# Optimization experiments

Hardware: AMD Instinct MI355X
Metric: run time of the kernel (lower is better)

Reference implementation:

```python
import jax, jax.numpy as jnp
import numpy as np

B, T = 64, 1024
VOCAB, EMBED, HIDDEN = 55, 64, 128


def setup_inputs() -> dict:
    key = jax.random.key(0)
    ks = jax.random.split(key, 15)
    stdv = 1.0 / np.sqrt(HIDDEN)
    u = lambda k, s: jax.random.uniform(k, s, jnp.float32, -stdv, stdv)
    return {
        "x": jax.random.randint(ks[0], (B, T), 0, VOCAB),
        "emb": jax.random.normal(ks[1], (VOCAB, EMBED), jnp.float32),
        "w_ih0": u(ks[2], (HIDDEN, EMBED)),
        "b_ih0": u(ks[3], (HIDDEN,)),
        "w_hh0": u(ks[4], (HIDDEN, HIDDEN)),
        "b_hh0": u(ks[5], (HIDDEN,)),
        "w_ih1": u(ks[6], (HIDDEN, HIDDEN)),
        "b_ih1": u(ks[7], (HIDDEN,)),
        "w_hh1": u(ks[8], (HIDDEN, HIDDEN)),
        "b_hh1": u(ks[9], (HIDDEN,)),
        "attn_w": u(ks[10], (HIDDEN, HIDDEN)),
        "attn_b": u(ks[11], (HIDDEN,)),
        "fc_w": u(ks[12], (VOCAB, 2 * HIDDEN)),
        "fc_b": u(ks[13], (VOCAB,)),
    }


def reference(x, emb, w_ih0, b_ih0, w_hh0, b_hh0, w_ih1, b_ih1, w_hh1, b_hh1,
              attn_w, attn_b, fc_w, fc_b):
    Bx, Tx = x.shape
    H = w_hh0.shape[0]
    e = emb[x]  # [B, T, E]

    def step(carry, x_t):  # x_t: [B, E]
        h0, h1 = carry
        h0 = jnp.tanh(x_t @ w_ih0.T + b_ih0 + h0 @ w_hh0.T + b_hh0)
        h1 = jnp.tanh(h0 @ w_ih1.T + b_ih1 + h1 @ w_hh1.T + b_hh1)
        return (h0, h1), h1

    init = (jnp.zeros((Bx, H), e.dtype), jnp.zeros((Bx, H), e.dtype))
    _, outs = jax.lax.scan(step, init, jnp.swapaxes(e, 0, 1))  # [T, B, H]
    outs = jnp.swapaxes(outs, 0, 1)  # [B, T, H]

    Q = outs @ attn_w.T + attn_b  # [B, T, H]
    scores = jnp.einsum('bth,bsh->bts', Q, outs) / jnp.sqrt(jnp.asarray(H, e.dtype))
    causal = jnp.tril(jnp.ones((Tx, Tx), bool))  # [T, T]
    scores = jnp.where(causal[None], scores, jnp.asarray(-jnp.inf, scores.dtype))
    attn = jax.nn.softmax(scores, axis=-1)
    context = jnp.einsum('bts,bsh->bth', attn, outs)  # [B, T, H]

    combined = jnp.concatenate([outs, context], axis=-1)  # [B, T, 2H]
    logits = combined @ fc_w.T + fc_b  # [B, T, vocab]
    return logits
```

## Files before the change

kernel.cpp:

```cpp
#include <hip/hip_runtime.h>
#include <hip/hip_bf16.h>
#include <cstdint>
#include <cstddef>


typedef __attribute__((ext_vector_type(8))) short short8;
typedef __attribute__((ext_vector_type(4))) float f32x4;

__device__ __forceinline__ float bf2f(unsigned short u) {
    union { unsigned int i; float f; } c; c.i = ((unsigned int)u) << 16; return c.f;
}
__device__ __forceinline__ unsigned short f2bf(float f) {
    union { float f; unsigned int i; } c; c.f = f;
    unsigned int u = c.i;
    u += 0x7fffu + ((u >> 16) & 1u);
    return (unsigned short)(u >> 16);
}
__device__ __forceinline__ unsigned int pk_bf16(float lo, float hi) {
    union { __hip_bfloat162 h2; unsigned int u; } c;
    c.h2 = __float22bfloat162_rn(make_float2(lo, hi));
    return c.u;
}
__device__ __forceinline__ float fast_tanh(float x) {
    float e = __expf(2.0f * x);
    return 1.0f - 2.0f * __builtin_amdgcn_rcpf(e + 1.0f);
}
__device__ __forceinline__ void bar_lds() {
    asm volatile("s_waitcnt lgkmcnt(0)\n\ts_barrier" ::: "memory");
}
__device__ __forceinline__ short8 ld_a_bf16(const float* p) {
    const float4* q = (const float4*)p;
    float4 f0 = q[0], f1 = q[1];
    short8 r;
    r[0]=(short)f2bf(f0.x); r[1]=(short)f2bf(f0.y);
    r[2]=(short)f2bf(f0.z); r[3]=(short)f2bf(f0.w);
    r[4]=(short)f2bf(f1.x); r[5]=(short)f2bf(f1.y);
    r[6]=(short)f2bf(f1.z); r[7]=(short)f2bf(f1.w);
    return r;
}
__device__ __forceinline__ void ld_fc_hilo(const float* p, short8& hi, short8& lo) {
    const float4* q = (const float4*)p;
    float4 f0 = q[0], f1 = q[1];
    float ff[8] = {f0.x, f0.y, f0.z, f0.w, f1.x, f1.y, f1.z, f1.w};
#pragma unroll
    for (int i = 0; i < 8; ++i) {
        unsigned short hb = f2bf(ff[i]);
        hi[i] = (short)hb;
        lo[i] = (short)f2bf(ff[i] - bf2f(hb));
    }
}

__global__ __launch_bounds__(128)
void k_we(const float* __restrict__ emb, const float* __restrict__ w_ih0,
          const float* __restrict__ b_ih0, const float* __restrict__ b_hh0,
          float* __restrict__ WE)
{
    __shared__ float ev[64];
    const int i = threadIdx.x;
    const int v = blockIdx.x;
    if (i < 64) ev[i] = emb[v * 64 + i];
    __syncthreads();
    float s = b_ih0[i] + b_hh0[i];
    const float* wr = w_ih0 + i * 64;
#pragma unroll
    for (int k = 0; k < 64; ++k) s += wr[k] * ev[k];
    WE[v * 128 + i] = s;
}

__global__ __launch_bounds__(256)
void k_weg(const int* __restrict__ x, const float* __restrict__ WE,
           float* __restrict__ WEg)
{
    __shared__ int xv[32];
    const int tid = threadIdx.x;
    const int b   = blockIdx.y;
    const int t0  = blockIdx.x * 32;
    if (tid < 32) xv[tid] = x[b * 1024 + t0 + tid];
    __syncthreads();
#pragma unroll
    for (int it = 0; it < 4; ++it) {
        int tt = it * 8 + (tid >> 5);
        int c4 = tid & 31;
        float4 v = ((const float4*)(WE + xv[tt] * 128))[c4];
        ((float4*)(WEg + ((size_t)b * 1024 + t0 + tt) * 128))[c4] = v;
    }
}

__global__ __launch_bounds__(512, 1)
void k_scan5(const float* __restrict__ WEg,
             const float* __restrict__ w_hh0,
             const float* __restrict__ w_ih1, const float* __restrict__ b_ih1,
             const float* __restrict__ w_hh1, const float* __restrict__ b_hh1,
             unsigned short* __restrict__ outs_bf)
{
    const int tid   = threadIdx.x;
    const int w     = tid >> 6;
    const int lane  = tid & 63;
    const int quad  = lane >> 4;
    const int n     = lane & 15;
    const int bbase = blockIdx.x * 16;

    __shared__ __align__(16) unsigned short h0buf[2][16][136];
    __shared__ __align__(16) unsigned short h1buf[2][16][136];

    if (w < 4) {
        const int r0 = w * 32 + quad * 4;
        const int r1 = r0 + 16;
        short8 a0[2][4];
#pragma unroll
        for (int r = 0; r < 2; ++r) {
            const size_t mrow = (size_t)(w * 32 + r * 16 + n) * 128;
#pragma unroll
            for (int ks = 0; ks < 4; ++ks)
                a0[r][ks] = ld_a_bf16(w_hh0 + mrow + ks * 32 + quad * 8);
        }
        const size_t wegB0 = (size_t)(bbase + n) * 131072 + r0;
        const size_t wegB1 = wegB0 + 16;
        {
            float4 p0 = *(const float4*)(WEg + wegB0);
            float4 p1 = *(const float4*)(WEg + wegB1);
            *(uint2*)&h0buf[0][n][r0] = make_uint2(
                pk_bf16(fast_tanh(p0.x), fast_tanh(p0.y)),
                pk_bf16(fast_tanh(p0.z), fast_tanh(p0.w)));
            *(uint2*)&h0buf[0][n][r1] = make_uint2(
                pk_bf16(fast_tanh(p1.x), fast_tanh(p1.y)),
                pk_bf16(fast_tanh(p1.z), fast_tanh(p1.w)));
        }
        float4 wA0 = *(const float4*)(WEg + wegB0 + 128);
        float4 wA1 = *(const float4*)(WEg + wegB1 + 128);
        float4 wB0 = *(const float4*)(WEg + wegB0 + 256);
        float4 wB1 = *(const float4*)(WEg + wegB1 + 256);
        float4 wC0 = *(const float4*)(WEg + wegB0 + 384);
        float4 wC1 = *(const float4*)(WEg + wegB1 + 384);
        __syncthreads();

        for (int t = 0; t < 1024; ++t) {
            const int p = t & 1;
            if (t < 1023) {
                const unsigned short* h0p = &h0buf[p][n][quad * 8];
                short8 bh[4];
#pragma unroll
                for (int ks = 0; ks < 4; ++ks)
                    bh[ks] = *(const short8*)(h0p + ks * 32);
                f32x4 c0 = (f32x4){wA0.x, wA0.y, wA0.z, wA0.w};
                f32x4 c1 = (f32x4){wA1.x, wA1.y, wA1.z, wA1.w};
#pragma unroll
                for (int ks = 0; ks < 4; ++ks) {
                    c0 = __builtin_amdgcn_mfma_f32_16x16x32_bf16(a0[0][ks], bh[ks], c0, 0,0,0);
                    c1 = __builtin_amdgcn_mfma_f32_16x16x32_bf16(a0[1][ks], bh[ks], c1, 0,0,0);
                }
                wA0 = wB0; wA1 = wB1; wB0 = wC0; wB1 = wC1;
                const size_t tpre = (size_t)((t + 4 < 1024) ? t + 4 : 1023) * 128;
                wC0 = *(const float4*)(WEg + wegB0 + tpre);
                wC1 = *(const float4*)(WEg + wegB1 + tpre);
                *(uint2*)&h0buf[p ^ 1][n][r0] = make_uint2(
                    pk_bf16(fast_tanh(c0[0]), fast_tanh(c0[1])),
                    pk_bf16(fast_tanh(c0[2]), fast_tanh(c0[3])));
                *(uint2*)&h0buf[p ^ 1][n][r1] = make_uint2(
                    pk_bf16(fast_tanh(c1[0]), fast_tanh(c1[1])),
                    pk_bf16(fast_tanh(c1[2]), fast_tanh(c1[3])));
            }
            bar_lds();
        }
    } else {
        const int w2 = w - 4;
        const int r0 = w2 * 32 + quad * 4;
        const int r1 = r0 + 16;
        short8 a1[2][4], a2[2][4];
#pragma unroll
        for (int r = 0; r < 2; ++r) {
            const size_t mrow = (size_t)(w2 * 32 + r * 16 + n) * 128;
#pragma unroll
            for (int ks = 0; ks < 4; ++ks) {
                a1[r][ks] = ld_a_bf16(w_ih1 + mrow + ks * 32 + quad * 8);
                a2[r][ks] = ld_a_bf16(w_hh1 + mrow + ks * 32 + quad * 8);
            }
        }
        f32x4 b1i[2];
#pragma unroll
        for (int r = 0; r < 2; ++r)
#pragma unroll
            for (int j = 0; j < 4; ++j) {
                int row = w2 * 32 + r * 16 + quad * 4 + j;
                b1i[r][j] = b_ih1[row] + b_hh1[row];
            }
        *(uint2*)&h1buf[0][n][r0] = make_uint2(0u, 0u);
        *(uint2*)&h1buf[0][n][r1] = make_uint2(0u, 0u);
        unsigned short* outp0 = outs_bf + (size_t)(bbase + n) * 131072 + r0;
        unsigned short* outp1 = outp0 + 16;
        __syncthreads();

        for (int t = 0; t < 1024; ++t) {
            const int p = t & 1;
            const unsigned short* h0p = &h0buf[p][n][quad * 8];
            const unsigned short* h1p = &h1buf[p][n][quad * 8];
            short8 bh0[4], bh1[4];
#pragma unroll
            for (int ks = 0; ks < 4; ++ks) {
                bh0[ks] = *(const short8*)(h0p + ks * 32);
                bh1[ks] = *(const short8*)(h1p + ks * 32);
            }
            f32x4 c0 = b1i[0], c1 = b1i[1];
            f32x4 d0 = (f32x4){0.f,0.f,0.f,0.f}, d1 = (f32x4){0.f,0.f,0.f,0.f};
#pragma unroll
            for (int ks = 0; ks < 4; ++ks) {
                c0 = __builtin_amdgcn_mfma_f32_16x16x32_bf16(a1[0][ks], bh0[ks], c0, 0,0,0);
                c1 = __builtin_amdgcn_mfma_f32_16x16x32_bf16(a1[1][ks], bh0[ks], c1, 0,0,0);
                d0 = __builtin_amdgcn_mfma_f32_16x16x32_bf16(a2[0][ks], bh1[ks], d0, 0,0,0);
                d1 = __builtin_amdgcn_mfma_f32_16x16x32_bf16(a2[1][ks], bh1[ks], d1, 0,0,0);
            }
            uint2 o0 = make_uint2(
                pk_bf16(fast_tanh(c0[0] + d0[0]), fast_tanh(c0[1] + d0[1])),
                pk_bf16(fast_tanh(c0[2] + d0[2]), fast_tanh(c0[3] + d0[3])));
            uint2 o1 = make_uint2(
                pk_bf16(fast_tanh(c1[0] + d1[0]), fast_tanh(c1[1] + d1[1])),
                pk_bf16(fast_tanh(c1[2] + d1[2]), fast_tanh(c1[3] + d1[3])));
            *(uint2*)&h1buf[p ^ 1][n][r0] = o0;
            *(uint2*)&h1buf[p ^ 1][n][r1] = o1;
            *(uint2*)(outp0 + (size_t)t * 128) = o0;
            *(uint2*)(outp1 + (size_t)t * 128) = o1;
            bar_lds();
        }
    }
}

__global__ __launch_bounds__(256)
void k_transpose(const unsigned short* __restrict__ outs_bf,
                 unsigned short* __restrict__ outsT)
{
    __shared__ unsigned short lt[128][130];
    const int tid = threadIdx.x;
    const int t0  = blockIdx.x * 128;
    const int b   = blockIdx.y;
    const unsigned int* src =
        (const unsigned int*)(outs_bf + ((size_t)b * 1024 + t0) * 128);
    for (int idx = tid; idx < 8192; idx += 256) {
        int tr = idx >> 6, h2 = idx & 63;
        unsigned int v = src[tr * 64 + h2];
        lt[tr][h2 * 2]     = (unsigned short)(v & 0xffffu);
        lt[tr][h2 * 2 + 1] = (unsigned short)(v >> 16);
    }
    __syncthreads();
    unsigned int* dst = (unsigned int*)(outsT + (size_t)b * 128 * 1024);
    for (int idx = tid; idx < 8192; idx += 256) {
        int h = idx >> 6, t2 = idx & 63;
        unsigned int v = (unsigned int)lt[t2 * 2][h] |
                         ((unsigned int)lt[t2 * 2 + 1][h] << 16);
        dst[h * 512 + (t0 >> 1) + t2] = v;
    }
}

__global__ __launch_bounds__(512, 1)
void k_attnfc(const unsigned short* __restrict__ outs_bf,
              const unsigned short* __restrict__ outsT,
              const float* __restrict__ attn_w, const float* __restrict__ attn_b,
              const float* __restrict__ fc_w, const float* __restrict__ fc_b,
              float* __restrict__ out)
{
    __shared__ __align__(16) unsigned char smem[100352];
    unsigned short* lK = (unsigned short*)smem;
    unsigned short* lV = (unsigned short*)(smem + 32768);
    unsigned short* lP = (unsigned short*)(smem + 65536);

    const int tid  = threadIdx.x;
    const int w    = tid >> 6;
    const int lane = tid & 63;
    const int quad = lane >> 4;
    const int n    = lane & 15;
    const int qt   = blockIdx.x;
    const int b    = blockIdx.y;
    unsigned short* lPw = lP + w * 2176;
    const float cscale = 0.08838834764831845f;

    const unsigned short* outsB = outs_bf + (size_t)b * 131072;
    const int qrow = qt * 128 + w * 16 + n;

    short8 bo[4];
#pragma unroll
    for (int ks = 0; ks < 4; ++ks)
        bo[ks] = *(const short8*)(outsB + (size_t)qrow * 128 + ks * 32 + quad * 8);
#pragma unroll
    for (int mt = 0; mt < 8; ++mt) {
        short8 aw[4];
#pragma unroll
        for (int ks = 0; ks < 4; ++ks)
            aw[ks] = ld_a_bf16(attn_w + (size_t)(mt * 16 + n) * 128 + ks * 32 + quad * 8);
        f32x4 cq;
#pragma unroll
        for (int r = 0; r < 4; ++r) cq[r] = attn_b[mt * 16 + quad * 4 + r];
#pragma unroll
        for (int ks = 0; ks < 4; ++ks)
            cq = __builtin_amdgcn_mfma_f32_16x16x32_bf16(aw[ks], bo[ks], cq, 0,0,0);
        *(uint2*)&lPw[n * 136 + mt * 16 + quad * 4] =
            make_uint2(pk_bf16(cq[0], cq[1]), pk_bf16(cq[2], cq[3]));
    }
    short8 qf[4];
#pragma unroll
    for (int ks = 0; ks < 4; ++ks)
        qf[ks] = *(const short8*)&lPw[n * 136 + ks * 32 + quad * 8];

    f32x4 accO[8];
#pragma unroll
    for (int dt = 0; dt < 8; ++dt) accO[dt] = (f32x4){0.f, 0.f, 0.f, 0.f};
    float mx = -1e30f, lsum = 0.f;

    for (int kt = 0; kt <= qt; ++kt) {
        __syncthreads();
        for (int c = tid; c < 2048; c += 512) {
            int row = c >> 4, k8 = c & 15;
            uint4 vk = *(const uint4*)(outsB + (size_t)(kt * 128 + row) * 128 + k8 * 8);
            *(uint4*)&lK[row * 128 + ((k8 ^ (row & 15)) << 3)] = vk;
            uint4 vv = *(const uint4*)(outsT + ((size_t)b * 128 + row) * 1024 +
                                       kt * 128 + k8 * 8);
            *(uint4*)&lV[row * 128 + ((k8 ^ (row & 15)) << 3)] = vv;
        }
        __syncthreads();
        f32x4 accS[8];
#pragma unroll
        for (int mt = 0; mt < 8; ++mt) {
            short8 af[4];
#pragma unroll
            for (int ks = 0; ks < 4; ++ks) {
                int r = mt * 16 + n;
                af[ks] = *(const short8*)&lK[r * 128 + (((ks * 4 + quad) ^ (r & 15)) << 3)];
            }
            f32x4 s = (f32x4){0.f, 0.f, 0.f, 0.f};
#pragma unroll
            for (int ks = 0; ks < 4; ++ks)
                s = __builtin_amdgcn_mfma_f32_16x16x32_bf16(af[ks], qf[ks], s, 0,0,0);
            accS[mt] = s;
        }
        if (kt == qt) {
            const int ql = w * 16 + n;
#pragma unroll
            for (int mt = 0; mt < 8; ++mt)
#pragma unroll
                for (int jv = 0; jv < 4; ++jv)
                    if (mt * 16 + quad * 4 + jv > ql) accS[mt][jv] = -1e30f;
        }
        float tmax = accS[0][0];
#pragma unroll
        for (int mt = 0; mt < 8; ++mt)
#pragma unroll
            for (int jv = 0; jv < 4; ++jv) tmax = fmaxf(tmax, accS[mt][jv]);
        tmax = fmaxf(tmax, __shfl_xor(tmax, 16));
        tmax = fmaxf(tmax, __shfl_xor(tmax, 32));
        float nm = fmaxf(mx, tmax);
        float alpha = __expf((mx - nm) * cscale);
        float ss = 0.f;
#pragma unroll
        for (int mt = 0; mt < 8; ++mt)
#pragma unroll
            for (int jv = 0; jv < 4; ++jv) {
                float p = __expf((accS[mt][jv] - nm) * cscale);
                accS[mt][jv] = p;
                ss += p;
            }
        ss += __shfl_xor(ss, 16);
        ss += __shfl_xor(ss, 32);
        lsum = lsum * alpha + ss;
        mx = nm;
#pragma unroll
        for (int mt = 0; mt < 8; ++mt)
            *(uint2*)&lPw[n * 136 + mt * 16 + quad * 4] = make_uint2(
                pk_bf16(accS[mt][0], accS[mt][1]),
                pk_bf16(accS[mt][2], accS[mt][3]));
#pragma unroll
        for (int dt = 0; dt < 8; ++dt)
#pragma unroll
            for (int jv = 0; jv < 4; ++jv) accO[dt][jv] *= alpha;
        short8 pf[4];
#pragma unroll
        for (int ks = 0; ks < 4; ++ks)
            pf[ks] = *(const short8*)&lPw[n * 136 + ks * 32 + quad * 8];
#pragma unroll
        for (int dt = 0; dt < 8; ++dt) {
            short8 vf[4];
#pragma unroll
            for (int ks = 0; ks < 4; ++ks) {
                int d = dt * 16 + n;
                vf[ks] = *(const short8*)&lV[d * 128 + (((ks * 4 + quad) ^ (d & 15)) << 3)];
            }
#pragma unroll
            for (int ks = 0; ks < 4; ++ks)
                accO[dt] = __builtin_amdgcn_mfma_f32_16x16x32_bf16(vf[ks], pf[ks], accO[dt], 0,0,0);
        }
    }
    {
        float inv = __builtin_amdgcn_rcpf(lsum);
#pragma unroll
        for (int dt = 0; dt < 8; ++dt)
            *(uint2*)&lPw[n * 136 + dt * 16 + quad * 4] = make_uint2(
                pk_bf16(accO[dt][0] * inv, accO[dt][1] * inv),
                pk_bf16(accO[dt][2] * inv, accO[dt][3] * inv));
    }
    short8 bC[4];
#pragma unroll
    for (int ks = 0; ks < 4; ++ks)
        bC[ks] = *(const short8*)&lPw[n * 136 + ks * 32 + quad * 8];
#pragma unroll
    for (int mt = 0; mt < 4; ++mt) {
        const int vrow = mt * 16 + n;
        f32x4 acc;
#pragma unroll
        for (int r = 0; r < 4; ++r) {
            int vv = mt * 16 + quad * 4 + r;
            acc[r] = (vv < 55) ? fc_b[vv] : 0.f;
        }
#pragma unroll
        for (int c = 0; c < 8; ++c) {
            short8 hi, lo;
            if (vrow < 55) {
                ld_fc_hilo(fc_w + (size_t)vrow * 256 + c * 32 + quad * 8, hi, lo);
            } else {
#pragma unroll
                for (int i = 0; i < 8; ++i) { hi[i] = 0; lo[i] = 0; }
            }
            short8 bb = (c < 4) ? bo[c] : bC[c - 4];
            acc = __builtin_amdgcn_mfma_f32_16x16x32_bf16(hi, bb, acc, 0,0,0);
            acc = __builtin_amdgcn_mfma_f32_16x16x32_bf16(lo, bb, acc, 0,0,0);
        }
#pragma unroll
        for (int r = 0; r < 4; ++r) {
            int vv = mt * 16 + quad * 4 + r;
            if (vv < 55)
                out[((size_t)b * 1024 + qrow) * 55 + vv] = acc[r];
        }
    }
}

extern "C" void kernel_launch(void* const* d_in, const int* in_sizes, int n_in,
                              void* d_out, int out_size, void* d_ws, size_t ws_size,
                              hipStream_t stream)
{
    const int*   x      = (const int*)d_in[0];
    const float* emb    = (const float*)d_in[1];
    const float* w_ih0  = (const float*)d_in[2];
    const float* b_ih0  = (const float*)d_in[3];
    const float* w_hh0  = (const float*)d_in[4];
    const float* b_hh0  = (const float*)d_in[5];
    const float* w_ih1  = (const float*)d_in[6];
    const float* b_ih1  = (const float*)d_in[7];
    const float* w_hh1  = (const float*)d_in[8];
    const float* b_hh1  = (const float*)d_in[9];
    const float* attn_w = (const float*)d_in[10];
    const float* attn_b = (const float*)d_in[11];
    const float* fc_w   = (const float*)d_in[12];
    const float* fc_b   = (const float*)d_in[13];
    float* out = (float*)d_out;

    char* ws = (char*)d_ws;
    unsigned short* outs_bf = (unsigned short*)(ws);
    unsigned short* outsT   = (unsigned short*)(ws + ((size_t)16 << 20));
    float*          WEp     = (float*)         (ws + ((size_t)32 << 20));
    float*          WEg     = (float*)         (ws + ((size_t)33 << 20));

    k_we<<<dim3(55), dim3(128), 0, stream>>>(emb, w_ih0, b_ih0, b_hh0, WEp);
    k_weg<<<dim3(32, 64), dim3(256), 0, stream>>>(x, WEp, WEg);
    k_scan5<<<dim3(4), dim3(512), 0, stream>>>(
        WEg, w_hh0, w_ih1, b_ih1, w_hh1, b_hh1, outs_bf);
    k_transpose<<<dim3(8, 64), dim3(256), 0, stream>>>(outs_bf, outsT);
    k_attnfc<<<dim3(8, 64), dim3(512), 0, stream>>>(
        outs_bf, outsT, attn_w, attn_b, fc_w, fc_b, out);
}
```

Baseline: 786.2 us.

## Fuse scan, transpose and attention into one kernel with flag-based streaming

Merges the recurrent scan, transpose and attention/FC kernels into a single launch. Four blocks run the scan and publish progress flags every 128 timesteps with release stores. The remaining blocks spin-wait on those flags with acquire loads, then transpose and run attention on each finished chunk, so downstream work overlaps the sequential scan. This relies on the scan blocks being scheduled before or alongside the waiting blocks, otherwise it can deadlock, and it adds fence and polling overhead.

```diff
diff --git a/kernel.cpp b/kernel.cpp
--- a/kernel.cpp
+++ b/kernel.cpp
@@ -48,6 +48,14 @@
         hi[i] = (short)hb;
         lo[i] = (short)f2bf(ff[i] - bf2f(hb));
     }
+}
+__device__ __forceinline__ void rel_store(int* p, int v) {
+    __threadfence();
+    __hip_atomic_store(p, v, __ATOMIC_RELEASE, __HIP_MEMORY_SCOPE_AGENT);
+}
+__device__ __forceinline__ void acq_wait_ge(int* p, int v) {
+    while (__hip_atomic_load(p, __ATOMIC_ACQUIRE, __HIP_MEMORY_SCOPE_AGENT) < v)
+        __builtin_amdgcn_s_sleep(64);
 }
 
 __global__ __launch_bounds__(128)
@@ -86,345 +94,370 @@
     }
 }
 
+__global__ __launch_bounds__(1024)
+void k_zero(int* __restrict__ f)
+{
+    if (threadIdx.x < 544) f[threadIdx.x] = 0;
+}
+
 __global__ __launch_bounds__(512, 1)
-void k_scan5(const float* __restrict__ WEg,
+void k_fused(const float* __restrict__ WEg,
              const float* __restrict__ w_hh0,
              const float* __restrict__ w_ih1, const float* __restrict__ b_ih1,
              const float* __restrict__ w_hh1, const float* __restrict__ b_hh1,
-             unsigned short* __restrict__ outs_bf)
-{
-    const int tid   = threadIdx.x;
-    const int w     = tid >> 6;
-    const int lane  = tid & 63;
-    const int quad  = lane >> 4;
-    const int n     = lane & 15;
-    const int bbase = blockIdx.x * 16;
-
-    __shared__ __align__(16) unsigned short h0buf[2][16][136];
-    __shared__ __align__(16) unsigned short h1buf[2][16][136];
-
-    if (w < 4) {
-        const int r0 = w * 32 + quad * 4;
-        const int r1 = r0 + 16;
-        short8 a0[2][4];
-#pragma unroll
-        for (int r = 0; r < 2; ++r) {
-            const size_t mrow = (size_t)(w * 32 + r * 16 + n) * 128;
-#pragma unroll
-            for (int ks = 0; ks < 4; ++ks)
-                a0[r][ks] = ld_a_bf16(w_hh0 + mrow + ks * 32 + quad * 8);
-        }
-        const size_t wegB0 = (size_t)(bbase + n) * 131072 + r0;
-        const size_t wegB1 = wegB0 + 16;
-        {
-            float4 p0 = *(const float4*)(WEg + wegB0);
-            float4 p1 = *(const float4*)(WEg + wegB1);
-            *(uint2*)&h0buf[0][n][r0] = make_uint2(
-                pk_bf16(fast_tanh(p0.x), fast_tanh(p0.y)),
-                pk_bf16(fast_tanh(p0.z), fast_tanh(p0.w)));
-            *(uint2*)&h0buf[0][n][r1] = make_uint2(
-                pk_bf16(fast_tanh(p1.x), fast_tanh(p1.y)),
-                pk_bf16(fast_tanh(p1.z), fast_tanh(p1.w)));
-        }
-        float4 wA0 = *(const float4*)(WEg + wegB0 + 128);
-        float4 wA1 = *(const float4*)(WEg + wegB1 + 128);
-        float4 wB0 = *(const float4*)(WEg + wegB0 + 256);
-        float4 wB1 = *(const float4*)(WEg + wegB1 + 256);
-        float4 wC0 = *(const float4*)(WEg + wegB0 + 384);
-        float4 wC1 = *(const float4*)(WEg + wegB1 + 384);
-        __syncthreads();
-
-        for (int t = 0; t < 1024; ++t) {
-            const int p = t & 1;
-            if (t < 1023) {
-                const unsigned short* h0p = &h0buf[p][n][quad * 8];
-                short8 bh[4];
-#pragma unroll
-                for (int ks = 0; ks < 4; ++ks)
-                    bh[ks] = *(const short8*)(h0p + ks * 32);
-                f32x4 c0 = (f32x4){wA0.x, wA0.y, wA0.z, wA0.w};
-                f32x4 c1 = (f32x4){wA1.x, wA1.y, wA1.z, wA1.w};
-#pragma unroll
-                for (int ks = 0; ks < 4; ++ks) {
-                    c0 = __builtin_amdgcn_mfma_f32_16x16x32_bf16(a0[0][ks], bh[ks], c0, 0,0,0);
-                    c1 = __builtin_amdgcn_mfma_f32_16x16x32_bf16(a0[1][ks], bh[ks], c1, 0,0,0);
-                }
-                wA0 = wB0; wA1 = wB1; wB0 = wC0; wB1 = wC1;
-                const size_t tpre = (size_t)((t + 4 < 1024) ? t + 4 : 1023) * 128;
-                wC0 = *(const float4*)(WEg + wegB0 + tpre);
-                wC1 = *(const float4*)(WEg + wegB1 + tpre);
-                *(uint2*)&h0buf[p ^ 1][n][r0] = make_uint2(
-                    pk_bf16(fast_tanh(c0[0]), fast_tanh(c0[1])),
-                    pk_bf16(fast_tanh(c0[2]), fast_tanh(c0[3])));
-                *(uint2*)&h0buf[p ^ 1][n][r1] = make_uint2(
-                    pk_bf16(fast_tanh(c1[0]), fast_tanh(c1[1])),
-                    pk_bf16(fast_tanh(c1[2]), fast_tanh(c1[3])));
-            }
-            bar_lds();
-        }
-    } else {
-        const int w2 = w - 4;
-        const int r0 = w2 * 32 + quad * 4;
-        const int r1 = r0 + 16;
-        short8 a1[2][4], a2[2][4];
-#pragma unroll
-        for (int r = 0; r < 2; ++r) {
-            const size_t mrow = (size_t)(w2 * 32 + r * 16 + n) * 128;
-#pragma unroll
-            for (int ks = 0; ks < 4; ++ks) {
-                a1[r][ks] = ld_a_bf16(w_ih1 + mrow + ks * 32 + quad * 8);
-                a2[r][ks] = ld_a_bf16(w_hh1 + mrow + ks * 32 + quad * 8);
-            }
-        }
-        f32x4 b1i[2];
-#pragma unroll
-        for (int r = 0; r < 2; ++r)
-#pragma unroll
-            for (int j = 0; j < 4; ++j) {
-                int row = w2 * 32 + r * 16 + quad * 4 + j;
-                b1i[r][j] = b_ih1[row] + b_hh1[row];
-            }
-        *(uint2*)&h1buf[0][n][r0] = make_uint2(0u, 0u);
-        *(uint2*)&h1buf[0][n][r1] = make_uint2(0u, 0u);
-        unsigned short* outp0 = outs_bf + (size_t)(bbase + n) * 131072 + r0;
-        unsigned short* outp1 = outp0 + 16;
-        __syncthreads();
-
-        for (int t = 0; t < 1024; ++t) {
-            const int p = t & 1;
-            const unsigned short* h0p = &h0buf[p][n][quad * 8];
-            const unsigned short* h1p = &h1buf[p][n][quad * 8];
-            short8 bh0[4], bh1[4];
-#pragma unroll
-            for (int ks = 0; ks < 4; ++ks) {
-                bh0[ks] = *(const short8*)(h0p + ks * 32);
-                bh1[ks] = *(const short8*)(h1p + ks * 32);
-            }
-            f32x4 c0 = b1i[0], c1 = b1i[1];
-            f32x4 d0 = (f32x4){0.f,0.f,0.f,0.f}, d1 = (f32x4){0.f,0.f,0.f,0.f};
-#pragma unroll
-            for (int ks = 0; ks < 4; ++ks) {
-                c0 = __builtin_amdgcn_mfma_f32_16x16x32_bf16(a1[0][ks], bh0[ks], c0, 0,0,0);
-                c1 = __builtin_amdgcn_mfma_f32_16x16x32_bf16(a1[1][ks], bh0[ks], c1, 0,0,0);
-                d0 = __builtin_amdgcn_mfma_f32_16x16x32_bf16(a2[0][ks], bh1[ks], d0, 0,0,0);
-                d1 = __builtin_amdgcn_mfma_f32_16x16x32_bf16(a2[1][ks], bh1[ks], d1, 0,0,0);
-            }
-            uint2 o0 = make_uint2(
-                pk_bf16(fast_tanh(c0[0] + d0[0]), fast_tanh(c0[1] + d0[1])),
-                pk_bf16(fast_tanh(c0[2] + d0[2]), fast_tanh(c0[3] + d0[3])));
-            uint2 o1 = make_uint2(
-                pk_bf16(fast_tanh(c1[0] + d1[0]), fast_tanh(c1[1] + d1[1])),
-                pk_bf16(fast_tanh(c1[2] + d1[2]), fast_tanh(c1[3] + d1[3])));
-            *(uint2*)&h1buf[p ^ 1][n][r0] = o0;
-            *(uint2*)&h1buf[p ^ 1][n][r1] = o1;
-            *(uint2*)(outp0 + (size_t)t * 128) = o0;
-            *(uint2*)(outp1 + (size_t)t * 128) = o1;
-            bar_lds();
-        }
-    }
-}
-
-__global__ __launch_bounds__(256)
-void k_transpose(const unsigned short* __restrict__ outs_bf,
-                 unsigned short* __restrict__ outsT)
-{
-    __shared__ unsigned short lt[128][130];
-    const int tid = threadIdx.x;
-    const int t0  = blockIdx.x * 128;
-    const int b   = blockIdx.y;
-    const unsigned int* src =
-        (const unsigned int*)(outs_bf + ((size_t)b * 1024 + t0) * 128);
-    for (int idx = tid; idx < 8192; idx += 256) {
-        int tr = idx >> 6, h2 = idx & 63;
-        unsigned int v = src[tr * 64 + h2];
-        lt[tr][h2 * 2]     = (unsigned short)(v & 0xffffu);
-        lt[tr][h2 * 2 + 1] = (unsigned short)(v >> 16);
-    }
-    __syncthreads();
-    unsigned int* dst = (unsigned int*)(outsT + (size_t)b * 128 * 1024);
-    for (int idx = tid; idx < 8192; idx += 256) {
-        int h = idx >> 6, t2 = idx & 63;
-        unsigned int v = (unsigned int)lt[t2 * 2][h] |
-                         ((unsigned int)lt[t2 * 2 + 1][h] << 16);
-        dst[h * 512 + (t0 >> 1) + t2] = v;
-    }
-}
-
-__global__ __launch_bounds__(512, 1)
-void k_attnfc(const unsigned short* __restrict__ outs_bf,
-              const unsigned short* __restrict__ outsT,
-              const float* __restrict__ attn_w, const float* __restrict__ attn_b,
-              const float* __restrict__ fc_w, const float* __restrict__ fc_b,
-              float* __restrict__ out)
+             unsigned short* __restrict__ outs_bf,
+             unsigned short* __restrict__ outsT,
+             const float* __restrict__ attn_w, const float* __restrict__ attn_b,
+             const float* __restrict__ fc_w, const float* __restrict__ fc_b,
+             float* __restrict__ out, int* __restrict__ flags)
 {
     __shared__ __align__(16) unsigned char smem[100352];
-    unsigned short* lK = (unsigned short*)smem;
-    unsigned short* lV = (unsigned short*)(smem + 32768);
-    unsigned short* lP = (unsigned short*)(smem + 65536);
-
+    const int bx   = blockIdx.x;
     const int tid  = threadIdx.x;
     const int w    = tid >> 6;
     const int lane = tid & 63;
     const int quad = lane >> 4;
     const int n    = lane & 15;
-    const int qt   = blockIdx.x;
-    const int b    = blockIdx.y;
-    unsigned short* lPw = lP + w * 2176;
-    const float cscale = 0.08838834764831845f;
-
-    const unsigned short* outsB = outs_bf + (size_t)b * 131072;
-    const int qrow = qt * 128 + w * 16 + n;
-
-    short8 bo[4];
-#pragma unroll
-    for (int ks = 0; ks < 4; ++ks)
-        bo[ks] = *(const short8*)(outsB + (size_t)qrow * 128 + ks * 32 + quad * 8);
-#pragma unroll
-    for (int mt = 0; mt < 8; ++mt) {
-        short8 aw[4];
+
+    if (bx < 4) {
+        typedef unsigned short (*HBuf)[16][136];
+        HBuf h0buf = (HBuf)(smem);
+        HBuf h1buf = (HBuf)(smem + 8704);
+        const int bbase = bx * 16;
+
+        if (w < 4) {
+            const int r0 = w * 32 + quad * 4;
+            const int r1 = r0 + 16;
+            short8 a0[2][4];
+#pragma unroll
+            for (int r = 0; r < 2; ++r) {
+                const size_t mrow = (size_t)(w * 32 + r * 16 + n) * 128;
+#pragma unroll
+                for (int ks = 0; ks < 4; ++ks)
+                    a0[r][ks] = ld_a_bf16(w_hh0 + mrow + ks * 32 + quad * 8);
+            }
+            const size_t wegB0 = (size_t)(bbase + n) * 131072 + r0;
+            const size_t wegB1 = wegB0 + 16;
+            {
+                float4 p0 = *(const float4*)(WEg + wegB0);
+                float4 p1 = *(const float4*)(WEg + wegB1);
+                *(uint2*)&h0buf[0][n][r0] = make_uint2(
+                    pk_bf16(fast_tanh(p0.x), fast_tanh(p0.y)),
+                    pk_bf16(fast_tanh(p0.z), fast_tanh(p0.w)));
+                *(uint2*)&h0buf[0][n][r1] = make_uint2(
+                    pk_bf16(fast_tanh(p1.x), fast_tanh(p1.y)),
+                    pk_bf16(fast_tanh(p1.z), fast_tanh(p1.w)));
+            }
+            float4 wA0 = *(const float4*)(WEg + wegB0 + 128);
+            float4 wA1 = *(const float4*)(WEg + wegB1 + 128);
+            float4 wB0 = *(const float4*)(WEg + wegB0 + 256);
+            float4 wB1 = *(const float4*)(WEg + wegB1 + 256);
+            float4 wC0 = *(const float4*)(WEg + wegB0 + 384);
+            float4 wC1 = *(const float4*)(WEg + wegB1 + 384);
+            __syncthreads();
+
+            for (int t = 0; t < 1024; ++t) {
+                const int p = t & 1;
+                if (t < 1023) {
+                    const unsigned short* h0p = &h0buf[p][n][quad * 8];
+                    short8 bh[4];
+#pragma unroll
+                    for (int ks = 0; ks < 4; ++ks)
+                        bh[ks] = *(const short8*)(h0p + ks * 32);
+                    f32x4 c0 = (f32x4){wA0.x, wA0.y, wA0.z, wA0.w};
+                    f32x4 c1 = (f32x4){wA1.x, wA1.y, wA1.z, wA1.w};
+#pragma unroll
+                    for (int ks = 0; ks < 4; ++ks) {
+                        c0 = __builtin_amdgcn_mfma_f32_16x16x32_bf16(a0[0][ks], bh[ks], c0, 0,0,0);
+                        c1 = __builtin_amdgcn_mfma_f32_16x16x32_bf16(a0[1][ks], bh[ks], c1, 0,0,0);
+                    }
+                    wA0 = wB0; wA1 = wB1; wB0 = wC0; wB1 = wC1;
+                    const size_t tpre = (size_t)((t + 4 < 1024) ? t + 4 : 1023) * 128;
+                    wC0 = *(const float4*)(WEg + wegB0 + tpre);
+                    wC1 = *(const float4*)(WEg + wegB1 + tpre);
+                    *(uint2*)&h0buf[p ^ 1][n][r0] = make_uint2(
+                        pk_bf16(fast_tanh(c0[0]), fast_tanh(c0[1])),
+                        pk_bf16(fast_tanh(c0[2]), fast_tanh(c0[3])));
+                    *(uint2*)&h0buf[p ^ 1][n][r1] = make_uint2(
+                        pk_bf16(fast_tanh(c1[0]), fast_tanh(c1[1])),
+                        pk_bf16(fast_tanh(c1[2]), fast_tanh(c1[3])));
+                }
+                bar_lds();
+                if ((t & 127) == 127) {
+                    asm volatile("s_waitcnt vmcnt(0)" ::: "memory");
+                    __syncthreads();
+                    if (tid == 0) rel_store(flags + bx, t + 1);
+                }
+            }
+        } else {
+            const int w2 = w - 4;
+            const int r0 = w2 * 32 + quad * 4;
+            const int r1 = r0 + 16;
+            short8 a1[2][4], a2[2][4];
+#pragma unroll
+            for (int r = 0; r < 2; ++r) {
+                const size_t mrow = (size_t)(w2 * 32 + r * 16 + n) * 128;
+#pragma unroll
+                for (int ks = 0; ks < 4; ++ks) {
+                    a1[r][ks] = ld_a_bf16(w_ih1 + mrow + ks * 32 + quad * 8);
+                    a2[r][ks] = ld_a_bf16(w_hh1 + mrow + ks * 32 + quad * 8);
+                }
+            }
+            f32x4 b1i[2];
+#pragma unroll
+            for (int r = 0; r < 2; ++r)
+#pragma unroll
+                for (int j = 0; j < 4; ++j) {
+                    int row = w2 * 32 + r * 16 + quad * 4 + j;
+                    b1i[r][j] = b_ih1[row] + b_hh1[row];
+                }
+            *(uint2*)&h1buf[0][n][r0] = make_uint2(0u, 0u);
+            *(uint2*)&h1buf[0][n][r1] = make_uint2(0u, 0u);
+            unsigned short* outp0 = outs_bf + (size_t)(bbase + n) * 131072 + r0;
+            unsigned short* outp1 = outp0 + 16;
+            __syncthreads();
+
+            for (int t = 0; t < 1024; ++t) {
+                const int p = t & 1;
+                const unsigned short* h0p = &h0buf[p][n][quad * 8];
+                const unsigned short* h1p = &h1buf[p][n][quad * 8];
+                short8 bh0[4], bh1[4];
+#pragma unroll
+                for (int ks = 0; ks < 4; ++ks) {
+                    bh0[ks] = *(const short8*)(h0p + ks * 32);
+                    bh1[ks] = *(const short8*)(h1p + ks * 32);
+                }
+                f32x4 c0 = b1i[0], c1 = b1i[1];
+                f32x4 d0 = (f32x4){0.f,0.f,0.f,0.f}, d1 = (f32x4){0.f,0.f,0.f,0.f};
+#pragma unroll
+                for (int ks = 0; ks < 4; ++ks) {
+                    c0 = __builtin_amdgcn_mfma_f32_16x16x32_bf16(a1[0][ks], bh0[ks], c0, 0,0,0);
+                    c1 = __builtin_amdgcn_mfma_f32_16x16x32_bf16(a1[1][ks], bh0[ks], c1, 0,0,0);
+                    d0 = __builtin_amdgcn_mfma_f32_16x16x32_bf16(a2[0][ks], bh1[ks], d0, 0,0,0);
+                    d1 = __builtin_amdgcn_mfma_f32_16x16x32_bf16(a2[1][ks], bh1[ks], d1, 0,0,0);
+                }
+                uint2 o0 = make_uint2(
+                    pk_bf16(fast_tanh(c0[0] + d0[0]), fast_tanh(c0[1] + d0[1])),
+                    pk_bf16(fast_tanh(c0[2] + d0[2]), fast_tanh(c0[3] + d0[3])));
+                uint2 o1 = make_uint2(
+                    pk_bf16(fast_tanh(c1[0] + d1[0]), fast_tanh(c1[1] + d1[1])),
+                    pk_bf16(fast_tanh(c1[2] + d1[2]), fast_tanh(c1[3] + d1[3])));
+                *(uint2*)&h1buf[p ^ 1][n][r0] = o0;
+                *(uint2*)&h1buf[p ^ 1][n][r1] = o1;
+                *(uint2*)(outp0 + (size_t)t * 128) = o0;
+                *(uint2*)(outp1 + (size_t)t * 128) = o1;
+                bar_lds();
+                if ((t & 127) == 127) {
+                    asm volatile("s_waitcnt vmcnt(0)" ::: "memory");
+                    __syncthreads();
+                    if (tid == 0) rel_store(flags + bx, t + 1);
+                }
+            }
+        }
+        return;
+    }
+
+    if (bx < 516) {
+        const int i     = bx - 4;
+        const int chunk = i >> 6;
+        const int b     = i & 63;
+        if (tid == 0) acq_wait_ge(flags + (b >> 4), (chunk + 1) * 128);
+        __syncthreads();
+
+        typedef unsigned short (*LT)[130];
+        LT lt = (LT)smem;
+        const int t0 = chunk * 128;
+        const unsigned int* src =
+            (const unsigned int*)(outs_bf + ((size_t)b * 1024 + t0) * 128);
+        for (int idx = tid; idx < 8192; idx += 512) {
+            int tr = idx >> 6, h2 = idx & 63;
+            unsigned int v = src[tr * 64 + h2];
+            lt[tr][h2 * 2]     = (unsigned short)(v & 0xffffu);
+            lt[tr][h2 * 2 + 1] = (unsigned short)(v >> 16);
+        }
+        __syncthreads();
+        unsigned int* dst = (unsigned int*)(outsT + (size_t)b * 131072);
+        for (int idx = tid; idx < 8192; idx += 512) {
+            int h = idx >> 6, t2 = idx & 63;
+            unsigned int v = (unsigned int)lt[t2 * 2][h] |
+                             ((unsigned int)lt[t2 * 2 + 1][h] << 16);
+            dst[h * 512 + (t0 >> 1) + t2] = v;
+        }
+        asm volatile("s_waitcnt vmcnt(0)" ::: "memory");
+        __syncthreads();
+        if (tid == 0) rel_store(flags + 16 + b * 8 + chunk, 1);
+        return;
+    }
+
+    {
+        const int i  = bx - 516;
+        const int qt = i >> 6;
+        const int b  = i & 63;
+        if (tid == 0) {
+            for (int c = 0; c <= qt; ++c) acq_wait_ge(flags + 16 + b * 8 + c, 1);
+        }
+        __syncthreads();
+
+        unsigned short* lK = (unsigned short*)smem;
+        unsigned short* lV = (unsigned short*)(smem + 32768);
+        unsigned short* lP = (unsigned short*)(smem + 65536);
+        unsigned short* lPw = lP + w * 2176;
+        const float cscale = 0.08838834764831845f;
+
+        const unsigned short* outsB = outs_bf + (size_t)b * 131072;
+        const int qrow = qt * 128 + w * 16 + n;
+
+        short8 bo[4];
 #pragma unroll
         for (int ks = 0; ks < 4; ++ks)
-            aw[ks] = ld_a_bf16(attn_w + (size_t)(mt * 16 + n) * 128 + ks * 32 + quad * 8);
-        f32x4 cq;
-#pragma unroll
-        for (int r = 0; r < 4; ++r) cq[r] = attn_b[mt * 16 + quad * 4 + r];
+            bo[ks] = *(const short8*)(outsB + (size_t)qrow * 128 + ks * 32 + quad * 8);
+#pragma unroll
+        for (int mt = 0; mt < 8; ++mt) {
+            short8 aw[4];
+#pragma unroll
+            for (int ks = 0; ks < 4; ++ks)
+                aw[ks] = ld_a_bf16(attn_w + (size_t)(mt * 16 + n) * 128 + ks * 32 + quad * 8);
+            f32x4 cq;
+#pragma unroll
+            for (int r = 0; r < 4; ++r) cq[r] = attn_b[mt * 16 + quad * 4 + r];
+#pragma unroll
+            for (int ks = 0; ks < 4; ++ks)
+                cq = __builtin_amdgcn_mfma_f32_16x16x32_bf16(aw[ks], bo[ks], cq, 0,0,0);
+            *(uint2*)&lPw[n * 136 + mt * 16 + quad * 4] =
+                make_uint2(pk_bf16(cq[0], cq[1]), pk_bf16(cq[2], cq[3]));
+        }
+        short8 qf[4];
 #pragma unroll
         for (int ks = 0; ks < 4; ++ks)
-            cq = __builtin_amdgcn_mfma_f32_16x16x32_bf16(aw[ks], bo[ks], cq, 0,0,0);
-        *(uint2*)&lPw[n * 136 + mt * 16 + quad * 4] =
-            make_uint2(pk_bf16(cq[0], cq[1]), pk_bf16(cq[2], cq[3]));
-    }
-    short8 qf[4];
-#pragma unroll
-    for (int ks = 0; ks < 4; ++ks)
-        qf[ks] = *(const short8*)&lPw[n * 136 + ks * 32 + quad * 8];
-
-    f32x4 accO[8];
-#pragma unroll
-    for (int dt = 0; dt < 8; ++dt) accO[dt] = (f32x4){0.f, 0.f, 0.f, 0.f};
-    float mx = -1e30f, lsum = 0.f;
-
-    for (int kt = 0; kt <= qt; ++kt) {
-        __syncthreads();
-        for (int c = tid; c < 2048; c += 512) {
-            int row = c >> 4, k8 = c & 15;
-            uint4 vk = *(const uint4*)(outsB + (size_t)(kt * 128 + row) * 128 + k8 * 8);
-            *(uint4*)&lK[row * 128 + ((k8 ^ (row & 15)) << 3)] = vk;
-            uint4 vv = *(const uint4*)(outsT + ((size_t)b * 128 + row) * 1024 +
-                                       kt * 128 + k8 * 8);
-            *(uint4*)&lV[row * 128 + ((k8 ^ (row & 15)) << 3)] = vv;
-        }
-        __syncthreads();
-        f32x4 accS[8];
-#pragma unroll
-        for (int mt = 0; mt < 8; ++mt) {
-            short8 af[4];
-#pragma unroll
-            for (int ks = 0; ks < 4; ++ks) {
-                int r = mt * 16 + n;
-                af[ks] = *(const short8*)&lK[r * 128 + (((ks * 4 + quad) ^ (r & 15)) << 3)];
-            }
-            f32x4 s = (f32x4){0.f, 0.f, 0.f, 0.f};
+            qf[ks] = *(const short8*)&lPw[n * 136 + ks * 32 + quad * 8];
+
+        f32x4 accO[8];
+#pragma unroll
+        for (int dt = 0; dt < 8; ++dt) accO[dt] = (f32x4){0.f, 0.f, 0.f, 0.f};
+        float mx = -1e30f, lsum = 0.f;
+
+        for (int kt = 0; kt <= qt; ++kt) {
+            __syncthreads();
+            for (int c = tid; c < 2048; c += 512) {
+                int row = c >> 4, k8 = c & 15;
+                uint4 vk = *(const uint4*)(outsB + (size_t)(kt * 128 + row) * 128 + k8 * 8);
+                *(uint4*)&lK[row * 128 + ((k8 ^ (row & 15)) << 3)] = vk;
+                uint4 vv = *(const uint4*)(outsT + ((size_t)b * 128 + row) * 1024 +
+                                           kt * 128 + k8 * 8);
+                *(uint4*)&lV[row * 128 + ((k8 ^ (row & 15)) << 3)] = vv;
+            }
+            __syncthreads();
+            f32x4 accS[8];
+#pragma unroll
+            for (int mt = 0; mt < 8; ++mt) {
+                short8 af[4];
+#pragma unroll
+                for (int ks = 0; ks < 4; ++ks) {
+                    int r = mt * 16 + n;
+                    af[ks] = *(const short8*)&lK[r * 128 + (((ks * 4 + quad) ^ (r & 15)) << 3)];
+                }
+                f32x4 s = (f32x4){0.f, 0.f, 0.f, 0.f};
+#pragma unroll
+                for (int ks = 0; ks < 4; ++ks)
+                    s = __builtin_amdgcn_mfma_f32_16x16x32_bf16(af[ks], qf[ks], s, 0,0,0);
+                accS[mt] = s;
+            }
+            if (kt == qt) {
+                const int ql = w * 16 + n;
+#pragma unroll
+                for (int mt = 0; mt < 8; ++mt)
+#pragma unroll
+                    for (int jv = 0; jv < 4; ++jv)
+                        if (mt * 16 + quad * 4 + jv > ql) accS[mt][jv] = -1e30f;
+            }
+            float tmax = accS[0][0];
+#pragma unroll
+            for (int mt = 0; mt < 8; ++mt)
+#pragma unroll
+                for (int jv = 0; jv < 4; ++jv) tmax = fmaxf(tmax, accS[mt][jv]);
+            tmax = fmaxf(tmax, __shfl_xor(tmax, 16));
+            tmax = fmaxf(tmax, __shfl_xor(tmax, 32));
+            float nm = fmaxf(mx, tmax);
+            float alpha = __expf((mx - nm) * cscale);
+            float ss = 0.f;
+#pragma unroll
+            for (int mt = 0; mt < 8; ++mt)
+#pragma unroll
+                for (int jv = 0; jv < 4; ++jv) {
+                    float p = __expf((accS[mt][jv] - nm) * cscale);
+                    accS[mt][jv] = p;
+                    ss += p;
+                }
+            ss += __shfl_xor(ss, 16);
+            ss += __shfl_xor(ss, 32);
+            lsum = lsum * alpha + ss;
+            mx = nm;
+#pragma unroll
+            for (int mt = 0; mt < 8; ++mt)
+                *(uint2*)&lPw[n * 136 + mt * 16 + quad * 4] = make_uint2(
+                    pk_bf16(accS[mt][0], accS[mt][1]),
+                    pk_bf16(accS[mt][2], accS[mt][3]));
+#pragma unroll
+            for (int dt = 0; dt < 8; ++dt)
+#pragma unroll
+                for (int jv = 0; jv < 4; ++jv) accO[dt][jv] *= alpha;
+            short8 pf[4];
 #pragma unroll
             for (int ks = 0; ks < 4; ++ks)
-                s = __builtin_amdgcn_mfma_f32_16x16x32_bf16(af[ks], qf[ks], s, 0,0,0);
-            accS[mt] = s;
-        }
-        if (kt == qt) {
-            const int ql = w * 16 + n;
-#pragma unroll
-            for (int mt = 0; mt < 8; ++mt)
-#pragma unroll
-                for (int jv = 0; jv < 4; ++jv)
-                    if (mt * 16 + quad * 4 + jv > ql) accS[mt][jv] = -1e30f;
-        }
-        float tmax = accS[0][0];
-#pragma unroll
-        for (int mt = 0; mt < 8; ++mt)
-#pragma unroll
-            for (int jv = 0; jv < 4; ++jv) tmax = fmaxf(tmax, accS[mt][jv]);
-        tmax = fmaxf(tmax, __shfl_xor(tmax, 16));
-        tmax = fmaxf(tmax, __shfl_xor(tmax, 32));
-        float nm = fmaxf(mx, tmax);
-        float alpha = __expf((mx - nm) * cscale);
-        float ss = 0.f;
-#pragma unroll
-        for (int mt = 0; mt < 8; ++mt)
-#pragma unroll
-            for (int jv = 0; jv < 4; ++jv) {
-                float p = __expf((accS[mt][jv] - nm) * cscale);
-                accS[mt][jv] = p;
-                ss += p;
-            }
-        ss += __shfl_xor(ss, 16);
-        ss += __shfl_xor(ss, 32);
-        lsum = lsum * alpha + ss;
-        mx = nm;
-#pragma unroll
-        for (int mt = 0; mt < 8; ++mt)
-            *(uint2*)&lPw[n * 136 + mt * 16 + quad * 4] = make_uint2(
-                pk_bf16(accS[mt][0], accS[mt][1]),
-                pk_bf16(accS[mt][2], accS[mt][3]));
-#pragma unroll
-        for (int dt = 0; dt < 8; ++dt)
-#pragma unroll
-            for (int jv = 0; jv < 4; ++jv) accO[dt][jv] *= alpha;
-        short8 pf[4];
+                pf[ks] = *(const short8*)&lPw[n * 136 + ks * 32 + quad * 8];
+#pragma unroll
+            for (int dt = 0; dt < 8; ++dt) {
+                short8 vf[4];
+#pragma unroll
+                for (int ks = 0; ks < 4; ++ks) {
+                    int d = dt * 16 + n;
+                    vf[ks] = *(const short8*)&lV[d * 128 + (((ks * 4 + quad) ^ (d & 15)) << 3)];
+                }
+#pragma unroll
+                for (int ks = 0; ks < 4; ++ks)
+                    accO[dt] = __builtin_amdgcn_mfma_f32_16x16x32_bf16(vf[ks], pf[ks], accO[dt], 0,0,0);
+            }
+        }
+        {
+            float inv = __builtin_amdgcn_rcpf(lsum);
+#pragma unroll
+            for (int dt = 0; dt < 8; ++dt)
+                *(uint2*)&lPw[n * 136 + dt * 16 + quad * 4] = make_uint2(
+                    pk_bf16(accO[dt][0] * inv, accO[dt][1] * inv),
+                    pk_bf16(accO[dt][2] * inv, accO[dt][3] * inv));
+        }
+        short8 bC[4];
 #pragma unroll
         for (int ks = 0; ks < 4; ++ks)
-            pf[ks] = *(const short8*)&lPw[n * 136 + ks * 32 + quad * 8];
-#pragma unroll
-        for (int dt = 0; dt < 8; ++dt) {
-            short8 vf[4];
-#pragma unroll
-            for (int ks = 0; ks < 4; ++ks) {
-                int d = dt * 16 + n;
-                vf[ks] = *(const short8*)&lV[d * 128 + (((ks * 4 + quad) ^ (d & 15)) << 3)];
-            }
-#pragma unroll
-            for (int ks = 0; ks < 4; ++ks)
-                accO[dt] = __builtin_amdgcn_mfma_f32_16x16x32_bf16(vf[ks], pf[ks], accO[dt], 0,0,0);
-        }
-    }
-    {
-        float inv = __builtin_amdgcn_rcpf(lsum);
-#pragma unroll
-        for (int dt = 0; dt < 8; ++dt)
-            *(uint2*)&lPw[n * 136 + dt * 16 + quad * 4] = make_uint2(
-                pk_bf16(accO[dt][0] * inv, accO[dt][1] * inv),
-                pk_bf16(accO[dt][2] * inv, accO[dt][3] * inv));
-    }
-    short8 bC[4];
-#pragma unroll
-    for (int ks = 0; ks < 4; ++ks)
-        bC[ks] = *(const short8*)&lPw[n * 136 + ks * 32 + quad * 8];
-#pragma unroll
-    for (int mt = 0; mt < 4; ++mt) {
-        const int vrow = mt * 16 + n;
-        f32x4 acc;
-#pragma unroll
-        for (int r = 0; r < 4; ++r) {
-            int vv = mt * 16 + quad * 4 + r;
-            acc[r] = (vv < 55) ? fc_b[vv] : 0.f;
-        }
-#pragma unroll
-        for (int c = 0; c < 8; ++c) {
-            short8 hi, lo;
-            if (vrow < 55) {
-                ld_fc_hilo(fc_w + (size_t)vrow * 256 + c * 32 + quad * 8, hi, lo);
-            } else {
-#pragma unroll
-                for (int i = 0; i < 8; ++i) { hi[i] = 0; lo[i] = 0; }
-            }
-            short8 bb = (c < 4) ? bo[c] : bC[c - 4];
-            acc = __builtin_amdgcn_mfma_f32_16x16x32_bf16(hi, bb, acc, 0,0,0);
-            acc = __builtin_amdgcn_mfma_f32_16x16x32_bf16(lo, bb, acc, 0,0,0);
-        }
-#pragma unroll
-        for (int r = 0; r < 4; ++r) {
-            int vv = mt * 16 + quad * 4 + r;
-            if (vv < 55)
-                out[((size_t)b * 1024 + qrow) * 55 + vv] = acc[r];
+            bC[ks] = *(const short8*)&lPw[n * 136 + ks * 32 + quad * 8];
+#pragma unroll
+        for (int mt = 0; mt < 4; ++mt) {
+            const int vrow = mt * 16 + n;
+            f32x4 acc;
+#pragma unroll
+            for (int r = 0; r < 4; ++r) {
+                int vv = mt * 16 + quad * 4 + r;
+                acc[r] = (vv < 55) ? fc_b[vv] : 0.f;
+            }
+#pragma unroll
+            for (int c = 0; c < 8; ++c) {
+                short8 hi, lo;
+                if (vrow < 55) {
+                    ld_fc_hilo(fc_w + (size_t)vrow * 256 + c * 32 + quad * 8, hi, lo);
+                } else {
+#pragma unroll
+                    for (int ii = 0; ii < 8; ++ii) { hi[ii] = 0; lo[ii] = 0; }
+                }
+                short8 bb = (c < 4) ? bo[c] : bC[c - 4];
+                acc = __builtin_amdgcn_mfma_f32_16x16x32_bf16(hi, bb, acc, 0,0,0);
+                acc = __builtin_amdgcn_mfma_f32_16x16x32_bf16(lo, bb, acc, 0,0,0);
+            }
+#pragma unroll
+            for (int r = 0; r < 4; ++r) {
+                int vv = mt * 16 + quad * 4 + r;
+                if (vv < 55)
+                    out[((size_t)b * 1024 + qrow) * 55 + vv] = acc[r];
+            }
         }
     }
 }
@@ -453,13 +486,13 @@
     unsigned short* outs_bf = (unsigned short*)(ws);
     unsigned short* outsT   = (unsigned short*)(ws + ((size_t)16 << 20));
     float*          WEp     = (float*)         (ws + ((size_t)32 << 20));
+    int*            flags   = (int*)           (ws + ((size_t)32 << 20) + (64 << 10));
     float*          WEg     = (float*)         (ws + ((size_t)33 << 20));
 
+    k_zero<<<dim3(1), dim3(1024), 0, stream>>>(flags);
     k_we<<<dim3(55), dim3(128), 0, stream>>>(emb, w_ih0, b_ih0, b_hh0, WEp);
     k_weg<<<dim3(32, 64), dim3(256), 0, stream>>>(x, WEp, WEg);
-    k_scan5<<<dim3(4), dim3(512), 0, stream>>>(
-        WEg, w_hh0, w_ih1, b_ih1, w_hh1, b_hh1, outs_bf);
-    k_transpose<<<dim3(8, 64), dim3(256), 0, stream>>>(outs_bf, outsT);
-    k_attnfc<<<dim3(8, 64), dim3(512), 0, stream>>>(
-        outs_bf, outsT, attn_w, attn_b, fc_w, fc_b, out);
-}
+    k_fused<<<dim3(1028), dim3(512), 0, stream>>>(
+        WEg, w_hh0, w_ih1, b_ih1, w_hh1, b_hh1, outs_bf, outsT,
+        attn_w, attn_b, fc_w, fc_b, out, flags);
+}
```

Result: slower. 1.225 ms (+55.8%).
